# Performance work log

Measured on AMD Instinct MI355X. Metric: run time of the kernel, lower is better.

The kernel has to match this reference:

```python
import jax, jax.numpy as jnp
import numpy as np


def setup_inputs() -> dict:
    key = jax.random.key(0)
    ks = jax.random.split(key, 5)
    B, N, L, d = 8, 2048, 2048, 512
    q = N // 4
    return {
        "logits": jax.random.normal(ks[0], (B, N, L), jnp.float32),
        "emb0": jax.random.normal(ks[1], (q, d), jnp.float32),
        "emb1": jax.random.normal(ks[2], (q, d), jnp.float32),
        "emb2": jax.random.normal(ks[3], (q, d), jnp.float32),
        "emb3": jax.random.normal(ks[4], (q, d), jnp.float32),
    }


def reference(logits, emb0, emb1, emb2, emb3):
    # Eval / late-epoch path of Embedding.forward (process_block_max, k=3):
    # per head: top-k over codebook dim -> masked softmax -> einsum combine.
    # softmax over only the top-k values is mathematically identical to
    # softmax of the -inf-masked full logits, and gathering the k codebook
    # rows is identical to the dense einsum 'bnl,nm->bml' with that sparse attn.
    K = 3
    B, N, L = logits.shape
    E = jnp.stack([emb0, emb1, emb2, emb3])            # (4, q, d)
    q = E.shape[1]
    lg = logits.reshape(B, 4, q, L).transpose(0, 1, 3, 2)  # (B, 4, L, q)
    vals, idx = jax.lax.top_k(lg, K)                   # (B, 4, L, K)
    w = jax.nn.softmax(vals, axis=-1)                  # sparse attn weights

    def head(emb_h, idx_h, w_h):
        g = emb_h[idx_h]                               # (B, L, K, d) gather
        return jnp.einsum('blk,blkd->bld', w_h, g)     # (B, L, d)

    outs = jax.vmap(head, in_axes=(0, 1, 1))(E, idx, w)  # (4, B, L, d)
    # output = out_0 + out_1 + out_2 + out_3, returned as (B, d, L)
    return outs.sum(axis=0).transpose(0, 2, 1)
```

## Files before the change

### kernel.cpp

```cpp
#include <hip/hip_runtime.h>
#include <math.h>

#define BB 8
#define NN 2048
#define LL 2048
#define QQ 512
#define DD 512

__device__ __forceinline__ void top3_insert(float v, int i, float& m0,
                                            float& m1, float& m2, int& j0,
                                            int& j1, int& j2) {
  bool gt0 = v > m0, gt1 = v > m1, gt2 = v > m2;
  float nv2 = gt1 ? m1 : (gt2 ? v : m2);
  int   ni2 = gt1 ? j1 : (gt2 ? i : j2);
  float nv1 = gt0 ? m0 : (gt1 ? v : m1);
  int   ni1 = gt0 ? j0 : (gt1 ? i : j1);
  m0 = gt0 ? v : m0;
  j0 = gt0 ? i : j0;
  m1 = nv1; j1 = ni1; m2 = nv2; j2 = ni2;
}

__global__ __launch_bounds__(256) void topk_part_kernel(
    const float* __restrict__ logits, float4* __restrict__ part) {
  const int u  = threadIdx.x & 63;
  const int g  = threadIdx.x >> 6;
  const int lt = blockIdx.x;
  const int h  = blockIdx.y;
  const int b  = blockIdx.z >> 2;
  const int ns = blockIdx.z & 3;
  const int l4 = lt * 256 + u * 4;
  const int n0 = ns * 128 + g * 32;

  const float* base = logits + ((size_t)(b * NN + h * QQ + n0) * LL) + l4;

  float v0[4], v1[4], v2[4];
  int   i0[4], i1[4], i2[4];
#pragma unroll
  for (int j = 0; j < 4; ++j) {
    v0[j] = v1[j] = v2[j] = -INFINITY;
    i0[j] = i1[j] = i2[j] = 0;
  }

  float4 buf[8];
  for (int t = 0; t < 4; ++t) {
#pragma unroll
    for (int p = 0; p < 8; ++p)
      buf[p] = *(const float4*)(base + (size_t)(t * 8 + p) * LL);
#pragma unroll
    for (int p = 0; p < 8; ++p) {
      const int i = n0 + t * 8 + p;
      top3_insert(buf[p].x, i, v0[0], v1[0], v2[0], i0[0], i1[0], i2[0]);
      top3_insert(buf[p].y, i, v0[1], v1[1], v2[1], i0[1], i1[1], i2[1]);
      top3_insert(buf[p].z, i, v0[2], v1[2], v2[2], i0[2], i1[2], i2[2]);
      top3_insert(buf[p].w, i, v0[3], v1[3], v2[3], i0[3], i1[3], i2[3]);
    }
  }

  __shared__ float sv[4][256][3];
  __shared__ int   si[4][256][3];
#pragma unroll
  for (int j = 0; j < 4; ++j) {
    const int ll = u * 4 + j;
    sv[g][ll][0] = v0[j]; sv[g][ll][1] = v1[j]; sv[g][ll][2] = v2[j];
    si[g][ll][0] = i0[j]; si[g][ll][1] = i1[j]; si[g][ll][2] = i2[j];
  }
  __syncthreads();

  const int t = threadIdx.x;
  float m0 = sv[0][t][0], m1 = sv[0][t][1], m2 = sv[0][t][2];
  int   j0 = si[0][t][0], j1 = si[0][t][1], j2 = si[0][t][2];
#pragma unroll
  for (int gg = 1; gg < 4; ++gg)
#pragma unroll
    for (int k = 0; k < 3; ++k)
      top3_insert(sv[gg][t][k], si[gg][t][k], m0, m1, m2, j0, j1, j2);

  unsigned int pi = (unsigned int)j0 | ((unsigned int)j1 << 9) |
                    ((unsigned int)j2 << 18);
  part[(size_t)(((b * 4 + h) * 4 + ns)) * LL + lt * 256 + t] =
      make_float4(m0, m1, m2, __uint_as_float(pi));
}

__global__ __launch_bounds__(256) void topk_merge_kernel(
    const float4* __restrict__ part, float4* __restrict__ wpack) {
  const int x   = blockIdx.x;
  const int bh  = x >> 3;
  const int l   = (x & 7) * 256 + threadIdx.x;
  const size_t base = (size_t)bh * 4 * LL + l;

  float4 P = part[base];
  float m0 = P.x, m1 = P.y, m2 = P.z;
  unsigned int pi = __float_as_uint(P.w);
  int j0 = pi & 511, j1 = (pi >> 9) & 511, j2 = (pi >> 18) & 511;
#pragma unroll
  for (int ns = 1; ns < 4; ++ns) {
    float4 Q = part[base + (size_t)ns * LL];
    unsigned int qi = __float_as_uint(Q.w);
    top3_insert(Q.x, qi & 511, m0, m1, m2, j0, j1, j2);
    top3_insert(Q.y, (qi >> 9) & 511, m0, m1, m2, j0, j1, j2);
    top3_insert(Q.z, (qi >> 18) & 511, m0, m1, m2, j0, j1, j2);
  }
  float e1 = __expf(m1 - m0), e2 = __expf(m2 - m0);
  float inv = 1.0f / (1.0f + e1 + e2);
  unsigned int po = (unsigned int)j0 | ((unsigned int)j1 << 9) |
                    ((unsigned int)j2 << 18);
  wpack[(size_t)bh * LL + l] =
      make_float4(inv, e1 * inv, e2 * inv, __uint_as_float(po));
}

__global__ __launch_bounds__(256) void combine_kernel(
    const float4* __restrict__ wpack,
    const float* __restrict__ emb0, const float* __restrict__ emb1,
    const float* __restrict__ emb2, const float* __restrict__ emb3,
    float* __restrict__ out) {
  const int u    = threadIdx.x & 63;
  const int w    = threadIdx.x >> 6;
  const int lblk = blockIdx.x * 16;
  const int b    = blockIdx.y;

  __shared__ float tile[16][516];

  const float* embs[4] = {emb0, emb1, emb2, emb3};

#pragma unroll
  for (int il = 0; il < 4; ++il) {
    const int l = lblk + w * 4 + il;
    float wt[12];
    const float* rows[12];
#pragma unroll
    for (int h = 0; h < 4; ++h) {
      float4 W = wpack[(size_t)(b * 4 + h) * LL + l];
      unsigned int pi = __float_as_uint(W.w);
      wt[h * 3 + 0] = W.x;
      wt[h * 3 + 1] = W.y;
      wt[h * 3 + 2] = W.z;
      rows[h * 3 + 0] = embs[h] + (size_t)(pi & 511) * DD;
      rows[h * 3 + 1] = embs[h] + (size_t)((pi >> 9) & 511) * DD;
      rows[h * 3 + 2] = embs[h] + (size_t)((pi >> 18) & 511) * DD;
    }
#pragma unroll
    for (int p = 0; p < 2; ++p) {
      const int d = p * 256 + u * 4;
      float a0 = 0.f, a1 = 0.f, a2 = 0.f, a3 = 0.f;
#pragma unroll
      for (int m = 0; m < 12; ++m) {
        const float4 e = *(const float4*)(rows[m] + d);
        a0 += wt[m] * e.x;
        a1 += wt[m] * e.y;
        a2 += wt[m] * e.z;
        a3 += wt[m] * e.w;
      }
      *(float4*)&tile[w * 4 + il][d] = make_float4(a0, a1, a2, a3);
    }
  }
  __syncthreads();

  const int l0  = (threadIdx.x & 3) * 4;
  const int dof = threadIdx.x >> 2;
  float* outb = out + (size_t)b * DD * LL + lblk + l0;
#pragma unroll
  for (int dd = 0; dd < 512; dd += 64) {
    const int d = dd + dof;
    float4 r;
    r.x = tile[l0 + 0][d];
    r.y = tile[l0 + 1][d];
    r.z = tile[l0 + 2][d];
    r.w = tile[l0 + 3][d];
    *(float4*)(outb + (size_t)d * LL) = r;
  }
}

extern "C" void kernel_launch(void* const* d_in, const int* in_sizes, int n_in,
                              void* d_out, int out_size, void* d_ws,
                              size_t ws_size, hipStream_t stream) {
  const float* logits = (const float*)d_in[0];
  const float* emb0   = (const float*)d_in[1];
  const float* emb1   = (const float*)d_in[2];
  const float* emb2   = (const float*)d_in[3];
  const float* emb3   = (const float*)d_in[4];
  float*       out    = (float*)d_out;

  float4* part  = (float4*)d_ws;
  float4* wpack = (float4*)((char*)d_ws + (size_t)8 * 4 * 4 * LL * 16);

  dim3 ga(8, 4, 32);
  topk_part_kernel<<<ga, 256, 0, stream>>>(logits, part);

  topk_merge_kernel<<<256, 256, 0, stream>>>(part, wpack);

  dim3 gb(LL / 16, BB);
  combine_kernel<<<gb, 256, 0, stream>>>(wpack, emb0, emb1, emb2, emb3, out);
}
```

Measured before the change: 234.2 us.

## Fuse top-k merge into combine kernel and drop LDS reduction in partial pass

The partial top-k kernel now writes one packed top-3 per 32-row chunk (16 chunks per head) directly to global memory, with no shared-memory reduction or barrier. The separate merge kernel is removed. The combine kernel now merges the 16 partials per (b,h,l) in 64 threads, computes the softmax weights, and stages them in LDS before gathering embedding rows. This removes one kernel launch and a global round-trip of the weights, at the cost of 4x more partial data written and read, plus a serial merge at the start of each combine block.

```diff
diff --git a/kernel.cpp b/kernel.cpp
--- a/kernel.cpp
+++ b/kernel.cpp
@@ -22,14 +22,15 @@
 
 __global__ __launch_bounds__(256) void topk_part_kernel(
     const float* __restrict__ logits, float4* __restrict__ part) {
-  const int u  = threadIdx.x & 63;
-  const int g  = threadIdx.x >> 6;
-  const int lt = blockIdx.x;
-  const int h  = blockIdx.y;
-  const int b  = blockIdx.z >> 2;
-  const int ns = blockIdx.z & 3;
-  const int l4 = lt * 256 + u * 4;
-  const int n0 = ns * 128 + g * 32;
+  const int u     = threadIdx.x & 63;
+  const int g     = threadIdx.x >> 6;
+  const int lt    = blockIdx.x;
+  const int h     = blockIdx.y;
+  const int b     = blockIdx.z >> 2;
+  const int ns    = blockIdx.z & 3;
+  const int chunk = ns * 4 + g;
+  const int n0    = chunk * 32;
+  const int l4    = lt * 256 + u * 4;
 
   const float* base = logits + ((size_t)(b * NN + h * QQ + n0) * LL) + l4;
 
@@ -56,60 +57,17 @@
     }
   }
 
-  __shared__ float sv[4][256][3];
-  __shared__ int   si[4][256][3];
+  float4* pout = part + ((size_t)((b * 4 + h) * 16 + chunk)) * LL + l4;
 #pragma unroll
   for (int j = 0; j < 4; ++j) {
-    const int ll = u * 4 + j;
-    sv[g][ll][0] = v0[j]; sv[g][ll][1] = v1[j]; sv[g][ll][2] = v2[j];
-    si[g][ll][0] = i0[j]; si[g][ll][1] = i1[j]; si[g][ll][2] = i2[j];
+    unsigned int pi = (unsigned int)i0[j] | ((unsigned int)i1[j] << 9) |
+                      ((unsigned int)i2[j] << 18);
+    pout[j] = make_float4(v0[j], v1[j], v2[j], __uint_as_float(pi));
   }
-  __syncthreads();
-
-  const int t = threadIdx.x;
-  float m0 = sv[0][t][0], m1 = sv[0][t][1], m2 = sv[0][t][2];
-  int   j0 = si[0][t][0], j1 = si[0][t][1], j2 = si[0][t][2];
-#pragma unroll
-  for (int gg = 1; gg < 4; ++gg)
-#pragma unroll
-    for (int k = 0; k < 3; ++k)
-      top3_insert(sv[gg][t][k], si[gg][t][k], m0, m1, m2, j0, j1, j2);
-
-  unsigned int pi = (unsigned int)j0 | ((unsigned int)j1 << 9) |
-                    ((unsigned int)j2 << 18);
-  part[(size_t)(((b * 4 + h) * 4 + ns)) * LL + lt * 256 + t] =
-      make_float4(m0, m1, m2, __uint_as_float(pi));
-}
-
-__global__ __launch_bounds__(256) void topk_merge_kernel(
-    const float4* __restrict__ part, float4* __restrict__ wpack) {
-  const int x   = blockIdx.x;
-  const int bh  = x >> 3;
-  const int l   = (x & 7) * 256 + threadIdx.x;
-  const size_t base = (size_t)bh * 4 * LL + l;
-
-  float4 P = part[base];
-  float m0 = P.x, m1 = P.y, m2 = P.z;
-  unsigned int pi = __float_as_uint(P.w);
-  int j0 = pi & 511, j1 = (pi >> 9) & 511, j2 = (pi >> 18) & 511;
-#pragma unroll
-  for (int ns = 1; ns < 4; ++ns) {
-    float4 Q = part[base + (size_t)ns * LL];
-    unsigned int qi = __float_as_uint(Q.w);
-    top3_insert(Q.x, qi & 511, m0, m1, m2, j0, j1, j2);
-    top3_insert(Q.y, (qi >> 9) & 511, m0, m1, m2, j0, j1, j2);
-    top3_insert(Q.z, (qi >> 18) & 511, m0, m1, m2, j0, j1, j2);
-  }
-  float e1 = __expf(m1 - m0), e2 = __expf(m2 - m0);
-  float inv = 1.0f / (1.0f + e1 + e2);
-  unsigned int po = (unsigned int)j0 | ((unsigned int)j1 << 9) |
-                    ((unsigned int)j2 << 18);
-  wpack[(size_t)bh * LL + l] =
-      make_float4(inv, e1 * inv, e2 * inv, __uint_as_float(po));
 }
 
 __global__ __launch_bounds__(256) void combine_kernel(
-    const float4* __restrict__ wpack,
+    const float4* __restrict__ part,
     const float* __restrict__ emb0, const float* __restrict__ emb1,
     const float* __restrict__ emb2, const float* __restrict__ emb3,
     float* __restrict__ out) {
@@ -118,25 +76,51 @@
   const int lblk = blockIdx.x * 16;
   const int b    = blockIdx.y;
 
+  __shared__ float wt_s[4][16][3];
+  __shared__ int   rid_s[4][16][3];
   __shared__ float tile[16][516];
+
+  if (threadIdx.x < 64) {
+    const int h  = threadIdx.x >> 4;
+    const int il = threadIdx.x & 15;
+    const int l  = lblk + il;
+    const float4* pp = part + ((size_t)(b * 4 + h) * 16) * LL + l;
+
+    float m0 = -INFINITY, m1 = -INFINITY, m2 = -INFINITY;
+    int   j0 = 0, j1 = 0, j2 = 0;
+#pragma unroll
+    for (int c = 0; c < 16; ++c) {
+      float4 P = pp[(size_t)c * LL];
+      unsigned int pi = __float_as_uint(P.w);
+      top3_insert(P.x, pi & 511, m0, m1, m2, j0, j1, j2);
+      top3_insert(P.y, (pi >> 9) & 511, m0, m1, m2, j0, j1, j2);
+      top3_insert(P.z, (pi >> 18) & 511, m0, m1, m2, j0, j1, j2);
+    }
+    float e1 = __expf(m1 - m0), e2 = __expf(m2 - m0);
+    float inv = 1.0f / (1.0f + e1 + e2);
+    wt_s[h][il][0] = inv;
+    wt_s[h][il][1] = e1 * inv;
+    wt_s[h][il][2] = e2 * inv;
+    rid_s[h][il][0] = j0;
+    rid_s[h][il][1] = j1;
+    rid_s[h][il][2] = j2;
+  }
+  __syncthreads();
 
   const float* embs[4] = {emb0, emb1, emb2, emb3};
 
 #pragma unroll
   for (int il = 0; il < 4; ++il) {
-    const int l = lblk + w * 4 + il;
+    const int ll = w * 4 + il;
     float wt[12];
     const float* rows[12];
 #pragma unroll
     for (int h = 0; h < 4; ++h) {
-      float4 W = wpack[(size_t)(b * 4 + h) * LL + l];
-      unsigned int pi = __float_as_uint(W.w);
-      wt[h * 3 + 0] = W.x;
-      wt[h * 3 + 1] = W.y;
-      wt[h * 3 + 2] = W.z;
-      rows[h * 3 + 0] = embs[h] + (size_t)(pi & 511) * DD;
-      rows[h * 3 + 1] = embs[h] + (size_t)((pi >> 9) & 511) * DD;
-      rows[h * 3 + 2] = embs[h] + (size_t)((pi >> 18) & 511) * DD;
+#pragma unroll
+      for (int k = 0; k < 3; ++k) {
+        wt[h * 3 + k]   = wt_s[h][ll][k];
+        rows[h * 3 + k] = embs[h] + (size_t)rid_s[h][ll][k] * DD;
+      }
     }
 #pragma unroll
     for (int p = 0; p < 2; ++p) {
@@ -150,7 +134,7 @@
         a2 += wt[m] * e.z;
         a3 += wt[m] * e.w;
       }
-      *(float4*)&tile[w * 4 + il][d] = make_float4(a0, a1, a2, a3);
+      *(float4*)&tile[ll][d] = make_float4(a0, a1, a2, a3);
     }
   }
   __syncthreads();
@@ -179,15 +163,11 @@
   const float* emb2   = (const float*)d_in[3];
   const float* emb3   = (const float*)d_in[4];
   float*       out    = (float*)d_out;
-
-  float4* part  = (float4*)d_ws;
-  float4* wpack = (float4*)((char*)d_ws + (size_t)8 * 4 * 4 * LL * 16);
+  float4*      part   = (float4*)d_ws;
 
   dim3 ga(8, 4, 32);
   topk_part_kernel<<<ga, 256, 0, stream>>>(logits, part);
 
-  topk_merge_kernel<<<256, 256, 0, stream>>>(part, wpack);
-
   dim3 gb(LL / 16, BB);
-  combine_kernel<<<gb, 256, 0, stream>>>(wpack, emb0, emb1, emb2, emb3, out);
+  combine_kernel<<<gb, 256, 0, stream>>>(part, emb0, emb1, emb2, emb3, out);
 }
```

Result: no change. 232.1 us (-0.9%).
